# Performance work log

Measured on AMD Instinct MI355X. Metric: run time of the kernel, lower is better.

## Reference

```python
import jax, jax.numpy as jnp
import numpy as np

B, C, H, W = 2, 64, 256, 256
DN = ('NCHW', 'OIHW', 'NCHW')


def _conv1x1(x, w, b):
    # x: [B,C,H,W], w: [O,C,1,1]
    return jnp.einsum('bchw,oc->bohw', x, w[:, :, 0, 0]) + b[None, :, None, None]


def _dw3x3(x, w, b):
    # depthwise 3x3, padding=1, groups=C; w: [C,1,3,3]
    y = jax.lax.conv_general_dilated(x, w, (1, 1), [(1, 1), (1, 1)],
                                     feature_group_count=x.shape[1],
                                     dimension_numbers=DN)
    return y + b[None, :, None, None]


def _proj(x, w1, b1, w2, b2):
    return _dw3x3(_conv1x1(x, w1, b1), w2, b2)


def _pixel_attention(initial, pattn1, pa_w, pa_b):
    b, c, h, w = initial.shape
    # interleave channels: [x_c0, p_c0, x_c1, p_c1, ...] per 'b c t h w -> b (c t) h w'
    x2 = jnp.stack([initial, pattn1], axis=2).reshape(b, 2 * c, h, w)
    x2 = jnp.pad(x2, ((0, 0), (0, 0), (3, 3), (3, 3)), mode='reflect')
    y = jax.lax.conv_general_dilated(x2, pa_w, (1, 1), 'VALID',
                                     feature_group_count=c,
                                     dimension_numbers=DN)
    return jax.nn.sigmoid(y + pa_b[None, :, None, None])


def setup_inputs() -> dict:
    key = jax.random.key(0)
    ks = jax.random.split(key, 26)

    def n(k, shape, s=0.05):
        return jax.random.normal(k, shape, dtype=jnp.float32) * s

    d = {
        'x_l': jax.random.normal(ks[0], (B, C, H, W), dtype=jnp.float32),
        'x_r': jax.random.normal(ks[1], (B, C, H, W), dtype=jnp.float32),
    }
    i = 2
    for pfx in ('lp1', 'rp1', 'lp2', 'rp2'):
        d[pfx + '_w1'] = n(ks[i], (C, C, 1, 1)); i += 1
        d[pfx + '_b1'] = n(ks[i], (C,)); i += 1
        d[pfx + '_w2'] = n(ks[i], (C, 1, 3, 3)); i += 1
        d[pfx + '_b2'] = n(ks[i], (C,)); i += 1
    for pfx in ('lp3', 'rp3'):
        d[pfx + '_w'] = n(ks[i], (C, C, 1, 1)); i += 1
        d[pfx + '_b'] = n(ks[i], (C,)); i += 1
    d['pa_w'] = n(ks[i], (C, 2, 7, 7)); i += 1
    d['pa_b'] = n(ks[i], (C,))
    return d


def reference(x_l, x_r,
              lp1_w1, lp1_b1, lp1_w2, lp1_b2,
              rp1_w1, rp1_b1, rp1_w2, rp1_b2,
              lp2_w1, lp2_b1, lp2_w2, lp2_b2,
              rp2_w1, rp2_b1, rp2_w2, rp2_b2,
              lp3_w, lp3_b, rp3_w, rp3_b,
              pa_w, pa_b):
    c = x_l.shape[1]
    scale = c ** (-0.5)
    initial = x_l + x_r

    # projections (1x1 conv + depthwise 3x3), then move channels last: [B,H,W,C]
    Q_l = _proj(x_l, lp1_w1, lp1_b1, lp1_w2, lp1_b2).transpose(0, 2, 3, 1)
    Q_r = _proj(x_r, rp1_w1, rp1_b1, rp1_w2, rp1_b2).transpose(0, 2, 3, 1)
    V_l = _proj(x_l, lp2_w1, lp2_b1, lp2_w2, lp2_b2).transpose(0, 2, 3, 1)
    V_r = _proj(x_r, rp2_w1, rp2_b1, rp2_w2, rp2_b2).transpose(0, 2, 3, 1)

    # cross-attention along the width axis per spatial row: [B,H,W,W]
    attn = jnp.einsum('bhwc,bhvc->bhwv', Q_l, Q_r) * scale
    F_r2l = jnp.einsum('bhwv,bhvc->bhwc', jax.nn.softmax(attn, axis=-1), V_r)
    F_l2r = jnp.einsum('bhwv,bhwc->bhvc', jax.nn.softmax(attn, axis=2), V_l)

    F_r2l = _conv1x1(F_r2l.transpose(0, 3, 1, 2), lp3_w, lp3_b)
    F_l2r = _conv1x1(F_l2r.transpose(0, 3, 1, 2), rp3_w, rp3_b)

    # PixelAttention returns sigmoid(...); EAGFM applies sigmoid again (faithful)
    a = jax.nn.sigmoid(_pixel_attention(initial, F_l2r + F_r2l, pa_w, pa_b))
    return a * x_l + (1.0 - a) * x_r
```

## Files before the change

### kernel.cpp

```cpp
#include <hip/hip_runtime.h>

typedef unsigned int uint;
typedef unsigned short ushort;
typedef _Float16 h2 __attribute__((ext_vector_type(2)));
typedef _Float16 f16x8 __attribute__((ext_vector_type(8)));
typedef float f32x4 __attribute__((ext_vector_type(4)));

#define HW 65536
#define W_ 256
#define H_ 256
#define C_ 64

__device__ __forceinline__ ushort f2hu(float f) { union { ushort u; _Float16 h; } x; x.h = (_Float16)f; return x.u; }
__device__ __forceinline__ float hu2f(ushort u) { union { ushort u; _Float16 h; } x; x.u = u; return (float)x.h; }

#define MFMA16(a, b, c) __builtin_amdgcn_mfma_f32_16x16x32_f16((a), (b), (c), 0, 0, 0)

__global__ __launch_bounds__(256) void wconv_k(const float* __restrict__ a0, const float* __restrict__ a1,
                                               const float* __restrict__ a2, const float* __restrict__ a3,
                                               const float* __restrict__ a4, const float* __restrict__ a5,
                                               ushort* __restrict__ dst) {
    int m = blockIdx.x;
    const float* src = m == 0 ? a0 : m == 1 ? a1 : m == 2 ? a2 : m == 3 ? a3 : m == 4 ? a4 : a5;
    ushort* d = dst + m * 4096;
    for (int i = threadIdx.x; i < 4096; i += 256) d[i] = f2hu(src[i]);
}

__global__ __launch_bounds__(256) void wpat_k(const float* __restrict__ pw, ushort* __restrict__ tbl) {
    int c = blockIdx.x;
    for (int i = threadIdx.x; i < 7168; i += 256) {
        int j = i & 7;
        int lane = (i >> 3) & 63;
        int f = i >> 9;
        int arr = f < 7 ? 0 : 1;
        int dy = f < 7 ? f : f - 7;
        int l15 = lane & 15, quad = lane >> 4;
        int k = quad * 8 + j;
        int t = k - l15 - 1;
        float v = (t >= 0 && t < 7) ? pw[c * 98 + arr * 49 + dy * 7 + t] : 0.0f;
        tbl[c * 7168 + i] = f2hu(v);
    }
}

__global__ __launch_bounds__(256, 2) void c1d_k(const float* __restrict__ x,
                                                const ushort* __restrict__ wfA,
                                                const float* __restrict__ biasA,
                                                ushort* __restrict__ yA,
                                                const ushort* __restrict__ wfB,
                                                const float* __restrict__ biasB,
                                                ushort* __restrict__ yB) {
    __shared__ ushort sY[64 * 264];
    int tid = threadIdx.x;
    int wv = tid >> 6, lane = tid & 63;
    int l15 = lane & 15, quad = lane >> 4;
    int pix0 = blockIdx.x * 256;
    int b = pix0 >> 16, hw0 = pix0 & 65535;
    const float* xb = x + ((size_t)b << 22) + hw0;

    f16x8 aX[4][2];
#pragma unroll
    for (int mt = 0; mt < 4; ++mt) {
        int pixl = wv * 64 + mt * 16 + l15;
#pragma unroll
        for (int kc = 0; kc < 2; ++kc) {
            f16x8 a;
#pragma unroll
            for (int j = 0; j < 8; ++j) {
                int c = kc * 32 + quad * 8 + j;
                a[j] = (_Float16)xb[((size_t)c << 16) + pixl];
            }
            aX[mt][kc] = a;
        }
    }

    for (int mat = 0; mat < 2; ++mat) {
        const ushort* wf = mat == 0 ? wfA : wfB;
        const float* bias = mat == 0 ? biasA : biasB;
        ushort* y = mat == 0 ? yA : yB;

        f16x8 bW[4][2];
#pragma unroll
        for (int nt = 0; nt < 4; ++nt)
#pragma unroll
            for (int kc = 0; kc < 2; ++kc)
                bW[nt][kc] = *(const f16x8*)(wf + (nt * 16 + l15) * 64 + kc * 32 + quad * 8);

        f32x4 acc[4][4];
#pragma unroll
        for (int mt = 0; mt < 4; ++mt)
#pragma unroll
            for (int nt = 0; nt < 4; ++nt) {
                f32x4 s = (f32x4)(0.0f);
                s = MFMA16(aX[mt][0], bW[nt][0], s);
                s = MFMA16(aX[mt][1], bW[nt][1], s);
                acc[mt][nt] = s;
            }

        if (mat == 1) __syncthreads();
#pragma unroll
        for (int nt = 0; nt < 4; ++nt) {
            int o = nt * 16 + l15;
            float bv = bias[o];
#pragma unroll
            for (int mt = 0; mt < 4; ++mt) {
                int pixl = wv * 64 + mt * 16 + quad * 4;
#pragma unroll
                for (int r = 0; r < 4; r += 2) {
                    h2 hh;
                    hh.x = (_Float16)(acc[mt][nt][r] + bv);
                    hh.y = (_Float16)(acc[mt][nt][r + 1] + bv);
                    *(h2*)&sY[o * 264 + pixl + r] = hh;
                }
            }
        }
        __syncthreads();
        ushort* yb = y + ((((size_t)b << 16) + hw0 + tid) << 6);
#pragma unroll
        for (int g = 0; g < 8; ++g) {
            ushort vs[8];
#pragma unroll
            for (int k = 0; k < 8; ++k) vs[k] = sY[(g * 8 + k) * 264 + tid];
            uint4 o;
            o.x = (uint)vs[0] | ((uint)vs[1] << 16);
            o.y = (uint)vs[2] | ((uint)vs[3] << 16);
            o.z = (uint)vs[4] | ((uint)vs[5] << 16);
            o.w = (uint)vs[6] | ((uint)vs[7] << 16);
            *(uint4*)(yb + g * 8) = o;
        }
    }
}

__global__ __launch_bounds__(256) void dwq_k(const ushort* __restrict__ xcl,
                                             const float* __restrict__ wgt,
                                             const float* __restrict__ bias,
                                             ushort* __restrict__ out) {
    __shared__ float sW[576];
    int tid = threadIdx.x;
    for (int i = tid; i < 576; i += 256) sW[i] = wgt[i];
    __syncthreads();
    int c = tid & 63, wq = tid >> 6;
    int wt = blockIdx.x, h = blockIdx.y, b = blockIdx.z;
    int wbase = wt * 64 + wq * 16;
    const float* wp = sW + c * 9;
    float bv = bias[c];
    float acc[16];
#pragma unroll
    for (int i = 0; i < 16; ++i) acc[i] = bv;
    size_t plane = (size_t)b << 16;
#pragma unroll
    for (int r = 0; r < 3; ++r) {
        int hh = h - 1 + r;
        int hhc = hh < 0 ? 0 : (hh > 255 ? 255 : hh);
        bool okh = (hh >= 0 && hh <= 255);
        float w0t = wp[r * 3], w1t = wp[r * 3 + 1], w2t = wp[r * 3 + 2];
        float v[18];
#pragma unroll
        for (int t = 0; t < 18; ++t) {
            int ww = wbase - 1 + t;
            int wwc = ww < 0 ? 0 : (ww > 255 ? 255 : ww);
            float xv = hu2f(xcl[((plane + (size_t)hhc * 256 + wwc) << 6) + c]);
            v[t] = (okh && ww >= 0 && ww <= 255) ? xv : 0.0f;
        }
#pragma unroll
        for (int i = 0; i < 16; ++i)
            acc[i] += w0t * v[i] + w1t * v[i + 1] + w2t * v[i + 2];
    }
    size_t obase = ((plane + (size_t)h * 256 + wbase) << 6) + c;
#pragma unroll
    for (int i = 0; i < 16; ++i)
        out[obase + ((size_t)i << 6)] = f2hu(acc[i]);
}

__global__ __launch_bounds__(256) void dwv_k(const ushort* __restrict__ xcl,
                                             const float* __restrict__ wgt,
                                             const float* __restrict__ bias,
                                             ushort* __restrict__ out) {
    __shared__ float sW[576];
    __shared__ ushort sT[64 * 66];
    int tid = threadIdx.x;
    for (int i = tid; i < 576; i += 256) sW[i] = wgt[i];
    __syncthreads();
    int c = tid & 63, wq = tid >> 6;
    int wt = blockIdx.x, h = blockIdx.y, b = blockIdx.z;
    int wbase = wt * 64 + wq * 16;
    const float* wp = sW + c * 9;
    float bv = bias[c];
    float acc[16];
#pragma unroll
    for (int i = 0; i < 16; ++i) acc[i] = bv;
    size_t plane = (size_t)b << 16;
#pragma unroll
    for (int r = 0; r < 3; ++r) {
        int hh = h - 1 + r;
        int hhc = hh < 0 ? 0 : (hh > 255 ? 255 : hh);
        bool okh = (hh >= 0 && hh <= 255);
        float w0t = wp[r * 3], w1t = wp[r * 3 + 1], w2t = wp[r * 3 + 2];
        float v[18];
#pragma unroll
        for (int t = 0; t < 18; ++t) {
            int ww = wbase - 1 + t;
            int wwc = ww < 0 ? 0 : (ww > 255 ? 255 : ww);
            float xv = hu2f(xcl[((plane + (size_t)hhc * 256 + wwc) << 6) + c]);
            v[t] = (okh && ww >= 0 && ww <= 255) ? xv : 0.0f;
        }
#pragma unroll
        for (int i = 0; i < 16; ++i)
            acc[i] += w0t * v[i] + w1t * v[i + 1] + w2t * v[i + 2];
    }
#pragma unroll
    for (int i = 0; i < 16; i += 2) {
        h2 hh2;
        hh2.x = (_Float16)acc[i];
        hh2.y = (_Float16)acc[i + 1];
        *(h2*)&sT[c * 66 + wq * 16 + i] = hh2;
    }
    __syncthreads();
    int cr = tid >> 2, ch = tid & 3;
    uint vb[8];
#pragma unroll
    for (int k = 0; k < 8; ++k) vb[k] = *(const uint*)&sT[cr * 66 + ch * 16 + k * 2];
    uint4 o0, o1;
    o0.x = vb[0]; o0.y = vb[1]; o0.z = vb[2]; o0.w = vb[3];
    o1.x = vb[4]; o1.y = vb[5]; o1.z = vb[6]; o1.w = vb[7];
    size_t bh16 = ((size_t)b * 256 + h) * 16384;
    ushort* ob = out + bh16 + (size_t)cr * 256 + wt * 64 + ch * 16;
    *(uint4*)ob = o0;
    *(uint4*)(ob + 8) = o1;
}

__global__ __launch_bounds__(256, 2) void att2_k(const ushort* __restrict__ Ql,
                                                 const ushort* __restrict__ Qr,
                                                 const ushort* __restrict__ Vl,
                                                 const ushort* __restrict__ Vr,
                                                 ushort* __restrict__ Fr2l,
                                                 ushort* __restrict__ Fl2r) {
    int bh = blockIdx.x;
    int tid = threadIdx.x;
    int wv = tid >> 6, lane = tid & 63;
    int l15 = lane & 15, quad = lane >> 4;
    __shared__ ushort sE[256 * 72];
    __shared__ ushort sEt[64 * 264];

    const ushort* qlb = Ql + (size_t)bh * 16384;
    const ushort* qrb = Qr + (size_t)bh * 16384;
    const ushort* vlb = Vl + (size_t)bh * 16384;
    const ushort* vrb = Vr + (size_t)bh * 16384;
    int p0 = wv * 64;
    int c0 = wv * 16;

    f16x8 aQ[4][2];
#pragma unroll
    for (int mt = 0; mt < 4; ++mt)
#pragma unroll
        for (int kc = 0; kc < 2; ++kc)
            aQ[mt][kc] = *(const f16x8*)(qlb + (p0 + mt * 16 + l15) * 64 + kc * 32 + quad * 8);

    f16x8 onesf;
#pragma unroll
    for (int i = 0; i < 8; ++i) onesf[i] = (_Float16)1.0f;

    f32x4 num1[4][4];
    f32x4 den[4];
#pragma unroll
    for (int mt = 0; mt < 4; ++mt) {
        den[mt] = (f32x4)(0.0f);
#pragma unroll
        for (int nt = 0; nt < 4; ++nt) num1[mt][nt] = (f32x4)(0.0f);
    }

    for (int kt = 0; kt < 4; ++kt) {
        int k0 = kt * 64;
        f32x4 S[4][4];
#pragma unroll
        for (int nt = 0; nt < 4; ++nt) {
            f16x8 bQ[2];
#pragma unroll
            for (int kc = 0; kc < 2; ++kc)
                bQ[kc] = *(const f16x8*)(qrb + (k0 + nt * 16 + l15) * 64 + kc * 32 + quad * 8);
#pragma unroll
            for (int mt = 0; mt < 4; ++mt) {
                f32x4 s = (f32x4)(0.0f);
                s = MFMA16(aQ[mt][0], bQ[0], s);
                s = MFMA16(aQ[mt][1], bQ[1], s);
                S[mt][nt] = s;
            }
        }
#pragma unroll
        for (int mt = 0; mt < 4; ++mt)
#pragma unroll
            for (int nt = 0; nt < 4; ++nt)
#pragma unroll
                for (int r = 0; r < 4; ++r)
                    S[mt][nt][r] = __expf(S[mt][nt][r] * 0.125f);

        __syncthreads();
#pragma unroll
        for (int mt = 0; mt < 4; ++mt)
#pragma unroll
            for (int nt = 0; nt < 4; ++nt)
#pragma unroll
                for (int r = 0; r < 4; ++r)
                    sE[(p0 + mt * 16 + quad * 4 + r) * 72 + nt * 16 + l15] = f2hu(S[mt][nt][r]);
#pragma unroll
        for (int mt = 0; mt < 4; ++mt)
#pragma unroll
            for (int nt = 0; nt < 4; ++nt)
#pragma unroll
            for (int pr = 0; pr < 4; pr += 2) {
                h2 hh;
                hh.x = (_Float16)S[mt][nt][pr];
                hh.y = (_Float16)S[mt][nt][pr + 1];
                *(h2*)&sEt[(nt * 16 + l15) * 264 + p0 + mt * 16 + quad * 4 + pr] = hh;
            }
        __syncthreads();

        f16x8 aE[4][2];
#pragma unroll
        for (int mt = 0; mt < 4; ++mt)
#pragma unroll
            for (int kc = 0; kc < 2; ++kc)
                aE[mt][kc] = *(const f16x8*)&sE[(p0 + mt * 16 + l15) * 72 + kc * 32 + quad * 8];
#pragma unroll
        for (int mt = 0; mt < 4; ++mt) {
            den[mt] = MFMA16(aE[mt][0], onesf, den[mt]);
            den[mt] = MFMA16(aE[mt][1], onesf, den[mt]);
        }
#pragma unroll
        for (int nt = 0; nt < 4; ++nt) {
            f16x8 bV[2];
#pragma unroll
            for (int kc = 0; kc < 2; ++kc)
                bV[kc] = *(const f16x8*)(vrb + (nt * 16 + l15) * 256 + k0 + kc * 32 + quad * 8);
#pragma unroll
            for (int mt = 0; mt < 4; ++mt) {
                num1[mt][nt] = MFMA16(aE[mt][0], bV[0], num1[mt][nt]);
                num1[mt][nt] = MFMA16(aE[mt][1], bV[1], num1[mt][nt]);
            }
        }
        f32x4 num2[4], den2[4];
#pragma unroll
        for (int mt = 0; mt < 4; ++mt) { num2[mt] = (f32x4)(0.0f); den2[mt] = (f32x4)(0.0f); }
        for (int pc = 0; pc < 8; ++pc) {
            f16x8 bL = *(const f16x8*)(vlb + (c0 + l15) * 256 + pc * 32 + quad * 8);
#pragma unroll
            for (int mt = 0; mt < 4; ++mt) {
                f16x8 aT = *(const f16x8*)&sEt[(mt * 16 + l15) * 264 + pc * 32 + quad * 8];
                num2[mt] = MFMA16(aT, bL, num2[mt]);
                den2[mt] = MFMA16(aT, onesf, den2[mt]);
            }
        }
#pragma unroll
        for (int mt = 0; mt < 4; ++mt)
#pragma unroll
            for (int r = 0; r < 4; ++r) {
                float v = num2[mt][r] * (1.0f / den2[mt][r]);
                Fl2r[(size_t)bh * 16384 + (k0 + mt * 16 + quad * 4 + r) * 64 + c0 + l15] = f2hu(v);
            }
    }
#pragma unroll
    for (int mt = 0; mt < 4; ++mt)
#pragma unroll
        for (int r = 0; r < 4; ++r) {
            float inv = 1.0f / den[mt][r];
#pragma unroll
            for (int nt = 0; nt < 4; ++nt) {
                float v = num1[mt][nt][r] * inv;
                Fr2l[(size_t)bh * 16384 + (p0 + mt * 16 + quad * 4 + r) * 64 + nt * 16 + l15] = f2hu(v);
            }
        }
}

__global__ __launch_bounds__(256, 2) void p3m_k(const ushort* __restrict__ F1,
                                                const ushort* __restrict__ F2,
                                                const ushort* __restrict__ wf1,
                                                const float* __restrict__ b1,
                                                const ushort* __restrict__ wf2,
                                                const float* __restrict__ b2,
                                                ushort* __restrict__ outp) {
    __shared__ ushort sY[64 * 264];
    int tid = threadIdx.x;
    int wv = tid >> 6, lane = tid & 63;
    int l15 = lane & 15, quad = lane >> 4;
    int pix0 = blockIdx.x * 256;
    int b = pix0 >> 16, hw0 = pix0 & 65535;

    f32x4 acc[4][4];
#pragma unroll
    for (int mt = 0; mt < 4; ++mt)
#pragma unroll
        for (int nt = 0; nt < 4; ++nt) acc[mt][nt] = (f32x4)(0.0f);

    for (int mat = 0; mat < 2; ++mat) {
        const ushort* F = mat == 0 ? F1 : F2;
        const ushort* wf = mat == 0 ? wf1 : wf2;
        f16x8 aF[4][2], bW[4][2];
#pragma unroll
        for (int mt = 0; mt < 4; ++mt) {
            int pixg = pix0 + wv * 64 + mt * 16 + l15;
#pragma unroll
            for (int kc = 0; kc < 2; ++kc)
                aF[mt][kc] = *(const f16x8*)(F + (size_t)pixg * 64 + kc * 32 + quad * 8);
        }
#pragma unroll
        for (int nt = 0; nt < 4; ++nt)
#pragma unroll
            for (int kc = 0; kc < 2; ++kc)
                bW[nt][kc] = *(const f16x8*)(wf + (nt * 16 + l15) * 64 + kc * 32 + quad * 8);
#pragma unroll
        for (int mt = 0; mt < 4; ++mt)
#pragma unroll
            for (int nt = 0; nt < 4; ++nt) {
                acc[mt][nt] = MFMA16(aF[mt][0], bW[nt][0], acc[mt][nt]);
                acc[mt][nt] = MFMA16(aF[mt][1], bW[nt][1], acc[mt][nt]);
            }
    }

#pragma unroll
    for (int nt = 0; nt < 4; ++nt) {
        int o = nt * 16 + l15;
        float bv = b1[o] + b2[o];
#pragma unroll
        for (int mt = 0; mt < 4; ++mt) {
            int pixl = wv * 64 + mt * 16 + quad * 4;
#pragma unroll
            for (int r = 0; r < 4; r += 2) {
                h2 hh;
                hh.x = (_Float16)(acc[mt][nt][r] + bv);
                hh.y = (_Float16)(acc[mt][nt][r + 1] + bv);
                *(h2*)&sY[o * 264 + pixl + r] = hh;
            }
        }
    }
    __syncthreads();
    ushort* yb = outp + ((size_t)b << 22) + hw0;
#pragma unroll
    for (int i = 0; i < 16; ++i) {
        int o = wv * 16 + i;
        uint2 v = *(const uint2*)&sY[o * 264 + lane * 4];
        *(uint2*)(yb + ((size_t)o << 16) + lane * 4) = v;
    }
}

__global__ __launch_bounds__(256, 4) void p4m_k(const float* __restrict__ x_l,
                                                const float* __restrict__ x_r,
                                                const ushort* __restrict__ pt,
                                                const ushort* __restrict__ tbl,
                                                const float* __restrict__ pb,
                                                float* __restrict__ out) {
    __shared__ ushort s_t[22 * 320];
    __shared__ ushort p_t[22 * 320];
    int tid = threadIdx.x;
    int tile = blockIdx.x & 15;
    int bc = blockIdx.x >> 4;
    int c = bc & 63;
    int h0 = tile << 4;
    size_t cbase = (size_t)bc << 16;

    {
        int a = tid & 127, rr = tid >> 7;
        int k = 2 * a + 4;
        int slotbase = (k >> 3);
        for (int pass = 0; pass < 11; ++pass) {
            int row = pass * 2 + rr;
            int hh = h0 + row - 3;
            hh = hh < 0 ? -hh : (hh > 255 ? 510 - hh : hh);
            size_t rb = cbase + ((size_t)hh << 8);
            float2 xl2 = *(const float2*)(x_l + rb + 2 * a);
            float2 xr2 = *(const float2*)(x_r + rb + 2 * a);
            uint pv = *(const uint*)(pt + rb + 2 * a);
            h2 sh;
            sh.x = (_Float16)(xl2.x + xr2.x);
            sh.y = (_Float16)(xl2.y + xr2.y);
            int off = row * 320 + (((slotbase ^ (row & 7)) << 3) | (k & 7));
            *(h2*)&s_t[off] = sh;
            *(uint*)&p_t[off] = pv;
        }
    }
    if (tid < 176) {
        int row = tid >> 3, g = tid & 7;
        int k = g < 2 ? g * 2 : (g < 4 ? 260 + (g - 2) * 2 : 264 + (g - 4) * 2);
        h2 sh; uint pv;
        if (g < 4) {
            int hh = h0 + row - 3;
            hh = hh < 0 ? -hh : (hh > 255 ? 510 - hh : hh);
            size_t rb = cbase + ((size_t)hh << 8);
            int w0 = k - 4, w1 = k - 3;
            int s0 = w0 < 0 ? -w0 : (w0 > 255 ? 510 - w0 : w0);
            int s1 = w1 < 0 ? -w1 : (w1 > 255 ? 510 - w1 : w1);
            sh.x = (_Float16)(x_l[rb + s0] + x_r[rb + s0]);
            sh.y = (_Float16)(x_l[rb + s1] + x_r[rb + s1]);
            pv = (uint)pt[rb + s0] | ((uint)pt[rb + s1] << 16);
        } else {
            sh.x = (_Float16)0.0f; sh.y = (_Float16)0.0f;
            pv = 0;
        }
        int off = row * 320 + ((((k >> 3) ^ (row & 7)) << 3) | (k & 7));
        *(h2*)&s_t[off] = sh;
        *(uint*)&p_t[off] = pv;
    }

    int wv = tid >> 6, lane = tid & 63;
    int l15 = lane & 15, quad = lane >> 4;
    const ushort* tb = tbl + c * 7168;
    f16x8 bW[14];
#pragma unroll
    for (int f = 0; f < 14; ++f)
        bW[f] = *(const f16x8*)(tb + (f * 64 + lane) * 8);

    float bias = pb[c];
    f32x4 acc[4];
#pragma unroll
    for (int t = 0; t < 4; ++t) acc[t] = (f32x4)(bias);

    __syncthreads();

#pragma unroll
    for (int f = 0; f < 14; ++f) {
        int dy = f < 7 ? f : f - 7;
        const ushort* tp = f < 7 ? s_t : p_t;
        int row = l15 + dy;
        int rbase = row * 320;
        int rx = row & 7;
#pragma unroll
        for (int t = 0; t < 4; ++t) {
            int L = wv * 8 + 2 * t + quad;
            f16x8 aF = *(const f16x8*)&tp[rbase + ((L ^ rx) << 3)];
            acc[t] = MFMA16(aF, bW[f], acc[t]);
        }
    }

    int hrow = h0 + quad * 4;
#pragma unroll
    for (int t = 0; t < 4; ++t) {
        int w = wv * 64 + t * 16 + l15;
#pragma unroll
        for (int r = 0; r < 4; ++r) {
            size_t idx = cbase + (size_t)(hrow + r) * 256 + w;
            float z = acc[t][r];
            float s1 = 1.0f / (1.0f + __expf(-z));
            float a  = 1.0f / (1.0f + __expf(-s1));
            float xl = x_l[idx], xr = x_r[idx];
            out[idx] = xr + a * (xl - xr);
        }
    }
}

extern "C" void kernel_launch(void* const* d_in, const int* in_sizes, int n_in,
                              void* d_out, int out_size, void* d_ws, size_t ws_size,
                              hipStream_t stream) {
    const float* x_l = (const float*)d_in[0];
    const float* x_r = (const float*)d_in[1];
    const float* lp1_w1 = (const float*)d_in[2];
    const float* lp1_b1 = (const float*)d_in[3];
    const float* lp1_w2 = (const float*)d_in[4];
    const float* lp1_b2 = (const float*)d_in[5];
    const float* rp1_w1 = (const float*)d_in[6];
    const float* rp1_b1 = (const float*)d_in[7];
    const float* rp1_w2 = (const float*)d_in[8];
    const float* rp1_b2 = (const float*)d_in[9];
    const float* lp2_w1 = (const float*)d_in[10];
    const float* lp2_b1 = (const float*)d_in[11];
    const float* lp2_w2 = (const float*)d_in[12];
    const float* lp2_b2 = (const float*)d_in[13];
    const float* rp2_w1 = (const float*)d_in[14];
    const float* rp2_b1 = (const float*)d_in[15];
    const float* rp2_w2 = (const float*)d_in[16];
    const float* rp2_b2 = (const float*)d_in[17];
    const float* lp3_w = (const float*)d_in[18];
    const float* lp3_b = (const float*)d_in[19];
    const float* rp3_w = (const float*)d_in[20];
    const float* rp3_b = (const float*)d_in[21];
    const float* pa_w = (const float*)d_in[22];
    const float* pa_b = (const float*)d_in[23];

    const size_t N = (size_t)2 * 64 * 256 * 256;
    char* ws = (char*)d_ws;
    ushort* tmpA = (ushort*)ws;
    ushort* wf16 = (ushort*)(ws + N * 2);
    ushort* tbl  = (ushort*)(ws + N * 2 + 6 * 4096 * 2);
    ushort* q_l   = (ushort*)(ws + N * 4);
    ushort* q_r   = q_l + N;
    ushort* v_l   = q_r + N;
    ushort* v_r   = v_l + N;
    ushort* f_r2l = v_r + N;
    ushort* f_l2r = f_r2l + N;
    ushort* tmpB  = f_l2r + N;

    dim3 blk(256);
    dim3 g_c1(512);
    dim3 g_dw(4, 256, 2);
    dim3 g_att(512);
    dim3 g_p3(512);
    dim3 g_p4(2048);

    wconv_k<<<6, blk, 0, stream>>>(lp1_w1, rp1_w1, lp2_w1, rp2_w1, lp3_w, rp3_w, wf16);
    wpat_k<<<64, blk, 0, stream>>>(pa_w, tbl);

    c1d_k<<<g_c1, blk, 0, stream>>>(x_l, wf16 + 0 * 4096, lp1_b1, tmpA, wf16 + 2 * 4096, lp2_b1, tmpB);
    dwq_k<<<g_dw, blk, 0, stream>>>(tmpA, lp1_w2, lp1_b2, q_l);
    dwv_k<<<g_dw, blk, 0, stream>>>(tmpB, lp2_w2, lp2_b2, v_l);

    c1d_k<<<g_c1, blk, 0, stream>>>(x_r, wf16 + 1 * 4096, rp1_b1, tmpA, wf16 + 3 * 4096, rp2_b1, tmpB);
    dwq_k<<<g_dw, blk, 0, stream>>>(tmpA, rp1_w2, rp1_b2, q_r);
    dwv_k<<<g_dw, blk, 0, stream>>>(tmpB, rp2_w2, rp2_b2, v_r);

    att2_k<<<g_att, blk, 0, stream>>>(q_l, q_r, v_l, v_r, f_r2l, f_l2r);

    p3m_k<<<g_p3, blk, 0, stream>>>(f_r2l, f_l2r, wf16 + 4 * 4096, lp3_b, wf16 + 5 * 4096, rp3_b, tmpA);

    p4m_k<<<g_p4, blk, 0, stream>>>(x_l, x_r, tmpA, tbl, pa_b, (float*)d_out);
}
```

Measured before the change: 323.2 us.

## Merge left/right 1x1 conv launches and split attention over 8 waves

The two per-side 1x1 conv launches are merged into one kernel with a 2D grid. Each side now writes to its own scratch buffers, so the depthwise kernels no longer wait behind each other on shared temporaries. The attention kernel moves from 256 to 512 threads per block: each wave handles 32 query rows instead of 64, and the transpose-side V product is split across wave halves. This halves per-wave register pressure and raises parallelism, at the cost of more workspace and more waves sharing the same LDS tiles and barriers.

```diff
diff --git a/kernel.cpp b/kernel.cpp
--- a/kernel.cpp
+++ b/kernel.cpp
@@ -42,14 +42,23 @@
     }
 }
 
-__global__ __launch_bounds__(256, 2) void c1d_k(const float* __restrict__ x,
-                                                const ushort* __restrict__ wfA,
-                                                const float* __restrict__ biasA,
-                                                ushort* __restrict__ yA,
-                                                const ushort* __restrict__ wfB,
-                                                const float* __restrict__ biasB,
-                                                ushort* __restrict__ yB) {
+__global__ __launch_bounds__(256, 2) void c1df_k(const float* __restrict__ xl,
+                                                 const float* __restrict__ xr,
+                                                 const ushort* __restrict__ wf16,
+                                                 const float* __restrict__ bA0, const float* __restrict__ bB0,
+                                                 const float* __restrict__ bA1, const float* __restrict__ bB1,
+                                                 ushort* __restrict__ y0A, ushort* __restrict__ y0B,
+                                                 ushort* __restrict__ y1A, ushort* __restrict__ y1B) {
     __shared__ ushort sY[64 * 264];
+    int side = blockIdx.y;
+    const float* x = side ? xr : xl;
+    const ushort* wfA = wf16 + side * 4096;
+    const ushort* wfB = wf16 + (2 + side) * 4096;
+    const float* biasA = side ? bA1 : bA0;
+    const float* biasB = side ? bB1 : bB0;
+    ushort* yAo = side ? y1A : y0A;
+    ushort* yBo = side ? y1B : y0B;
+
     int tid = threadIdx.x;
     int wv = tid >> 6, lane = tid & 63;
     int l15 = lane & 15, quad = lane >> 4;
@@ -76,7 +85,7 @@
     for (int mat = 0; mat < 2; ++mat) {
         const ushort* wf = mat == 0 ? wfA : wfB;
         const float* bias = mat == 0 ? biasA : biasB;
-        ushort* y = mat == 0 ? yA : yB;
+        ushort* y = mat == 0 ? yAo : yBo;
 
         f16x8 bW[4][2];
 #pragma unroll
@@ -228,12 +237,12 @@
     *(uint4*)(ob + 8) = o1;
 }
 
-__global__ __launch_bounds__(256, 2) void att2_k(const ushort* __restrict__ Ql,
-                                                 const ushort* __restrict__ Qr,
-                                                 const ushort* __restrict__ Vl,
-                                                 const ushort* __restrict__ Vr,
-                                                 ushort* __restrict__ Fr2l,
-                                                 ushort* __restrict__ Fl2r) {
+__global__ __launch_bounds__(512, 2) void att2x_k(const ushort* __restrict__ Ql,
+                                                  const ushort* __restrict__ Qr,
+                                                  const ushort* __restrict__ Vl,
+                                                  const ushort* __restrict__ Vr,
+                                                  ushort* __restrict__ Fr2l,
+                                                  ushort* __restrict__ Fl2r) {
     int bh = blockIdx.x;
     int tid = threadIdx.x;
     int wv = tid >> 6, lane = tid & 63;
@@ -245,12 +254,14 @@
     const ushort* qrb = Qr + (size_t)bh * 16384;
     const ushort* vlb = Vl + (size_t)bh * 16384;
     const ushort* vrb = Vr + (size_t)bh * 16384;
-    int p0 = wv * 64;
-    int c0 = wv * 16;
-
-    f16x8 aQ[4][2];
-#pragma unroll
-    for (int mt = 0; mt < 4; ++mt)
+    int p0 = wv * 32;
+    int vh = wv >> 2;
+    int cq = wv & 3;
+    int c0 = cq * 16;
+
+    f16x8 aQ[2][2];
+#pragma unroll
+    for (int mt = 0; mt < 2; ++mt)
 #pragma unroll
         for (int kc = 0; kc < 2; ++kc)
             aQ[mt][kc] = *(const f16x8*)(qlb + (p0 + mt * 16 + l15) * 64 + kc * 32 + quad * 8);
@@ -259,10 +270,10 @@
 #pragma unroll
     for (int i = 0; i < 8; ++i) onesf[i] = (_Float16)1.0f;
 
-    f32x4 num1[4][4];
-    f32x4 den[4];
-#pragma unroll
-    for (int mt = 0; mt < 4; ++mt) {
+    f32x4 num1[2][4];
+    f32x4 den[2];
+#pragma unroll
+    for (int mt = 0; mt < 2; ++mt) {
         den[mt] = (f32x4)(0.0f);
 #pragma unroll
         for (int nt = 0; nt < 4; ++nt) num1[mt][nt] = (f32x4)(0.0f);
@@ -270,7 +281,7 @@
 
     for (int kt = 0; kt < 4; ++kt) {
         int k0 = kt * 64;
-        f32x4 S[4][4];
+        f32x4 S[2][4];
 #pragma unroll
         for (int nt = 0; nt < 4; ++nt) {
             f16x8 bQ[2];
@@ -278,7 +289,7 @@
             for (int kc = 0; kc < 2; ++kc)
                 bQ[kc] = *(const f16x8*)(qrb + (k0 + nt * 16 + l15) * 64 + kc * 32 + quad * 8);
 #pragma unroll
-            for (int mt = 0; mt < 4; ++mt) {
+            for (int mt = 0; mt < 2; ++mt) {
                 f32x4 s = (f32x4)(0.0f);
                 s = MFMA16(aQ[mt][0], bQ[0], s);
                 s = MFMA16(aQ[mt][1], bQ[1], s);
@@ -286,7 +297,7 @@
             }
         }
 #pragma unroll
-        for (int mt = 0; mt < 4; ++mt)
+        for (int mt = 0; mt < 2; ++mt)
 #pragma unroll
             for (int nt = 0; nt < 4; ++nt)
 #pragma unroll
@@ -295,14 +306,14 @@
 
         __syncthreads();
 #pragma unroll
-        for (int mt = 0; mt < 4; ++mt)
+        for (int mt = 0; mt < 2; ++mt)
 #pragma unroll
             for (int nt = 0; nt < 4; ++nt)
 #pragma unroll
                 for (int r = 0; r < 4; ++r)
                     sE[(p0 + mt * 16 + quad * 4 + r) * 72 + nt * 16 + l15] = f2hu(S[mt][nt][r]);
 #pragma unroll
-        for (int mt = 0; mt < 4; ++mt)
+        for (int mt = 0; mt < 2; ++mt)
 #pragma unroll
             for (int nt = 0; nt < 4; ++nt)
 #pragma unroll
@@ -314,14 +325,14 @@
             }
         __syncthreads();
 
-        f16x8 aE[4][2];
-#pragma unroll
-        for (int mt = 0; mt < 4; ++mt)
+        f16x8 aE[2][2];
+#pragma unroll
+        for (int mt = 0; mt < 2; ++mt)
 #pragma unroll
             for (int kc = 0; kc < 2; ++kc)
                 aE[mt][kc] = *(const f16x8*)&sE[(p0 + mt * 16 + l15) * 72 + kc * 32 + quad * 8];
 #pragma unroll
-        for (int mt = 0; mt < 4; ++mt) {
+        for (int mt = 0; mt < 2; ++mt) {
             den[mt] = MFMA16(aE[mt][0], onesf, den[mt]);
             den[mt] = MFMA16(aE[mt][1], onesf, den[mt]);
         }
@@ -332,33 +343,33 @@
             for (int kc = 0; kc < 2; ++kc)
                 bV[kc] = *(const f16x8*)(vrb + (nt * 16 + l15) * 256 + k0 + kc * 32 + quad * 8);
 #pragma unroll
-            for (int mt = 0; mt < 4; ++mt) {
+            for (int mt = 0; mt < 2; ++mt) {
                 num1[mt][nt] = MFMA16(aE[mt][0], bV[0], num1[mt][nt]);
                 num1[mt][nt] = MFMA16(aE[mt][1], bV[1], num1[mt][nt]);
             }
         }
-        f32x4 num2[4], den2[4];
-#pragma unroll
-        for (int mt = 0; mt < 4; ++mt) { num2[mt] = (f32x4)(0.0f); den2[mt] = (f32x4)(0.0f); }
+        f32x4 num2[2], den2[2];
+#pragma unroll
+        for (int mt = 0; mt < 2; ++mt) { num2[mt] = (f32x4)(0.0f); den2[mt] = (f32x4)(0.0f); }
         for (int pc = 0; pc < 8; ++pc) {
             f16x8 bL = *(const f16x8*)(vlb + (c0 + l15) * 256 + pc * 32 + quad * 8);
 #pragma unroll
-            for (int mt = 0; mt < 4; ++mt) {
-                f16x8 aT = *(const f16x8*)&sEt[(mt * 16 + l15) * 264 + pc * 32 + quad * 8];
+            for (int mt = 0; mt < 2; ++mt) {
+                f16x8 aT = *(const f16x8*)&sEt[(vh * 32 + mt * 16 + l15) * 264 + pc * 32 + quad * 8];
                 num2[mt] = MFMA16(aT, bL, num2[mt]);
                 den2[mt] = MFMA16(aT, onesf, den2[mt]);
             }
         }
 #pragma unroll
-        for (int mt = 0; mt < 4; ++mt)
+        for (int mt = 0; mt < 2; ++mt)
 #pragma unroll
             for (int r = 0; r < 4; ++r) {
                 float v = num2[mt][r] * (1.0f / den2[mt][r]);
-                Fl2r[(size_t)bh * 16384 + (k0 + mt * 16 + quad * 4 + r) * 64 + c0 + l15] = f2hu(v);
-            }
-    }
-#pragma unroll
-    for (int mt = 0; mt < 4; ++mt)
+                Fl2r[(size_t)bh * 16384 + (k0 + vh * 32 + mt * 16 + quad * 4 + r) * 64 + c0 + l15] = f2hu(v);
+            }
+    }
+#pragma unroll
+    for (int mt = 0; mt < 2; ++mt)
 #pragma unroll
         for (int r = 0; r < 4; ++r) {
             float inv = 1.0f / den[mt][r];
@@ -575,7 +586,7 @@
 
     const size_t N = (size_t)2 * 64 * 256 * 256;
     char* ws = (char*)d_ws;
-    ushort* tmpA = (ushort*)ws;
+    ushort* clA0 = (ushort*)ws;
     ushort* wf16 = (ushort*)(ws + N * 2);
     ushort* tbl  = (ushort*)(ws + N * 2 + 6 * 4096 * 2);
     ushort* q_l   = (ushort*)(ws + N * 4);
@@ -584,10 +595,12 @@
     ushort* v_r   = v_l + N;
     ushort* f_r2l = v_r + N;
     ushort* f_l2r = f_r2l + N;
-    ushort* tmpB  = f_l2r + N;
+    ushort* clB0  = f_l2r + N;
+    ushort* clA1  = clB0 + N;
+    ushort* clB1  = clA1 + N;
 
     dim3 blk(256);
-    dim3 g_c1(512);
+    dim3 g_c1(512, 2);
     dim3 g_dw(4, 256, 2);
     dim3 g_att(512);
     dim3 g_p3(512);
@@ -596,17 +609,17 @@
     wconv_k<<<6, blk, 0, stream>>>(lp1_w1, rp1_w1, lp2_w1, rp2_w1, lp3_w, rp3_w, wf16);
     wpat_k<<<64, blk, 0, stream>>>(pa_w, tbl);
 
-    c1d_k<<<g_c1, blk, 0, stream>>>(x_l, wf16 + 0 * 4096, lp1_b1, tmpA, wf16 + 2 * 4096, lp2_b1, tmpB);
-    dwq_k<<<g_dw, blk, 0, stream>>>(tmpA, lp1_w2, lp1_b2, q_l);
-    dwv_k<<<g_dw, blk, 0, stream>>>(tmpB, lp2_w2, lp2_b2, v_l);
-
-    c1d_k<<<g_c1, blk, 0, stream>>>(x_r, wf16 + 1 * 4096, rp1_b1, tmpA, wf16 + 3 * 4096, rp2_b1, tmpB);
-    dwq_k<<<g_dw, blk, 0, stream>>>(tmpA, rp1_w2, rp1_b2, q_r);
-    dwv_k<<<g_dw, blk, 0, stream>>>(tmpB, rp2_w2, rp2_b2, v_r);
-
-    att2_k<<<g_att, blk, 0, stream>>>(q_l, q_r, v_l, v_r, f_r2l, f_l2r);
-
-    p3m_k<<<g_p3, blk, 0, stream>>>(f_r2l, f_l2r, wf16 + 4 * 4096, lp3_b, wf16 + 5 * 4096, rp3_b, tmpA);
-
-    p4m_k<<<g_p4, blk, 0, stream>>>(x_l, x_r, tmpA, tbl, pa_b, (float*)d_out);
-}
+    c1df_k<<<g_c1, blk, 0, stream>>>(x_l, x_r, wf16,
+                                     lp1_b1, lp2_b1, rp1_b1, rp2_b1,
+                                     clA0, clB0, clA1, clB1);
+    dwq_k<<<g_dw, blk, 0, stream>>>(clA0, lp1_w2, lp1_b2, q_l);
+    dwq_k<<<g_dw, blk, 0, stream>>>(clA1, rp1_w2, rp1_b2, q_r);
+    dwv_k<<<g_dw, blk, 0, stream>>>(clB0, lp2_w2, lp2_b2, v_l);
+    dwv_k<<<g_dw, blk, 0, stream>>>(clB1, rp2_w2, rp2_b2, v_r);
+
+    att2x_k<<<g_att, dim3(512), 0, stream>>>(q_l, q_r, v_l, v_r, f_r2l, f_l2r);
+
+    p3m_k<<<g_p3, blk, 0, stream>>>(f_r2l, f_l2r, wf16 + 4 * 4096, lp3_b, wf16 + 5 * 4096, rp3_b, clA0);
+
+    p4m_k<<<g_p4, blk, 0, stream>>>(x_l, x_r, clA0, tbl, pa_b, (float*)d_out);
+}
```

Result: slower. 331.1 us (+2.4%).

## Merge left/right projection launches and compute four rows per depthwise block

Applied to the files above, without the earlier changes.

Combines the left and right 1x1 conv launches into one grid and the two depthwise launches into single kernels indexed by side. Each depthwise block now produces four output rows from six loaded input rows, reusing loaded rows across adjacent outputs. This aims to cut redundant global loads and launch overhead. It uses extra workspace buffers and more registers per thread.

```diff
diff --git a/kernel.cpp b/kernel.cpp
--- a/kernel.cpp
+++ b/kernel.cpp
@@ -42,14 +42,23 @@
     }
 }
 
-__global__ __launch_bounds__(256, 2) void c1d_k(const float* __restrict__ x,
-                                                const ushort* __restrict__ wfA,
-                                                const float* __restrict__ biasA,
-                                                ushort* __restrict__ yA,
-                                                const ushort* __restrict__ wfB,
-                                                const float* __restrict__ biasB,
-                                                ushort* __restrict__ yB) {
+__global__ __launch_bounds__(256, 2) void c1df_k(const float* __restrict__ xl,
+                                                 const float* __restrict__ xr,
+                                                 const ushort* __restrict__ wf16,
+                                                 const float* __restrict__ bA0, const float* __restrict__ bB0,
+                                                 const float* __restrict__ bA1, const float* __restrict__ bB1,
+                                                 ushort* __restrict__ y0A, ushort* __restrict__ y0B,
+                                                 ushort* __restrict__ y1A, ushort* __restrict__ y1B) {
     __shared__ ushort sY[64 * 264];
+    int side = blockIdx.y;
+    const float* x = side ? xr : xl;
+    const ushort* wfA = wf16 + side * 4096;
+    const ushort* wfB = wf16 + (2 + side) * 4096;
+    const float* biasA = side ? bA1 : bA0;
+    const float* biasB = side ? bB1 : bB0;
+    ushort* yAo = side ? y1A : y0A;
+    ushort* yBo = side ? y1B : y0B;
+
     int tid = threadIdx.x;
     int wv = tid >> 6, lane = tid & 63;
     int l15 = lane & 15, quad = lane >> 4;
@@ -76,7 +85,7 @@
     for (int mat = 0; mat < 2; ++mat) {
         const ushort* wf = mat == 0 ? wfA : wfB;
         const float* bias = mat == 0 ? biasA : biasB;
-        ushort* y = mat == 0 ? yA : yB;
+        ushort* y = mat == 0 ? yAo : yBo;
 
         f16x8 bW[4][2];
 #pragma unroll
@@ -130,29 +139,36 @@
     }
 }
 
-__global__ __launch_bounds__(256) void dwq_k(const ushort* __restrict__ xcl,
-                                             const float* __restrict__ wgt,
-                                             const float* __restrict__ bias,
-                                             ushort* __restrict__ out) {
+__global__ __launch_bounds__(256) void dwq2_k(const ushort* __restrict__ x0, const ushort* __restrict__ x1,
+                                              const float* __restrict__ w0, const float* __restrict__ w1,
+                                              const float* __restrict__ b0, const float* __restrict__ b1,
+                                              ushort* __restrict__ o0, ushort* __restrict__ o1) {
+    int z = blockIdx.z;
+    int side = z >> 1, b = z & 1;
+    const ushort* xcl = side ? x1 : x0;
+    const float* wgt = side ? w1 : w0;
+    const float* bias = side ? b1 : b0;
+    ushort* out = side ? o1 : o0;
     __shared__ float sW[576];
     int tid = threadIdx.x;
     for (int i = tid; i < 576; i += 256) sW[i] = wgt[i];
     __syncthreads();
     int c = tid & 63, wq = tid >> 6;
-    int wt = blockIdx.x, h = blockIdx.y, b = blockIdx.z;
+    int wt = blockIdx.x, h0 = blockIdx.y * 4;
     int wbase = wt * 64 + wq * 16;
     const float* wp = sW + c * 9;
     float bv = bias[c];
-    float acc[16];
-#pragma unroll
-    for (int i = 0; i < 16; ++i) acc[i] = bv;
+    float acc[4][16];
+#pragma unroll
+    for (int o = 0; o < 4; ++o)
+#pragma unroll
+        for (int i = 0; i < 16; ++i) acc[o][i] = bv;
     size_t plane = (size_t)b << 16;
 #pragma unroll
-    for (int r = 0; r < 3; ++r) {
-        int hh = h - 1 + r;
+    for (int r = 0; r < 6; ++r) {
+        int hh = h0 - 1 + r;
         int hhc = hh < 0 ? 0 : (hh > 255 ? 255 : hh);
         bool okh = (hh >= 0 && hh <= 255);
-        float w0t = wp[r * 3], w1t = wp[r * 3 + 1], w2t = wp[r * 3 + 2];
         float v[18];
 #pragma unroll
         for (int t = 0; t < 18; ++t) {
@@ -162,39 +178,56 @@
             v[t] = (okh && ww >= 0 && ww <= 255) ? xv : 0.0f;
         }
 #pragma unroll
+        for (int o = 0; o < 4; ++o) {
+            if (o >= r - 2 && o <= r) {
+                int wr = r - o;
+                float wa = wp[wr * 3], wb = wp[wr * 3 + 1], wc2 = wp[wr * 3 + 2];
+#pragma unroll
+                for (int i = 0; i < 16; ++i)
+                    acc[o][i] += wa * v[i] + wb * v[i + 1] + wc2 * v[i + 2];
+            }
+        }
+    }
+#pragma unroll
+    for (int o = 0; o < 4; ++o) {
+        size_t obase = ((plane + (size_t)(h0 + o) * 256 + wbase) << 6) + c;
+#pragma unroll
         for (int i = 0; i < 16; ++i)
-            acc[i] += w0t * v[i] + w1t * v[i + 1] + w2t * v[i + 2];
-    }
-    size_t obase = ((plane + (size_t)h * 256 + wbase) << 6) + c;
-#pragma unroll
-    for (int i = 0; i < 16; ++i)
-        out[obase + ((size_t)i << 6)] = f2hu(acc[i]);
-}
-
-__global__ __launch_bounds__(256) void dwv_k(const ushort* __restrict__ xcl,
-                                             const float* __restrict__ wgt,
-                                             const float* __restrict__ bias,
-                                             ushort* __restrict__ out) {
+            out[obase + ((size_t)i << 6)] = f2hu(acc[o][i]);
+    }
+}
+
+__global__ __launch_bounds__(256) void dwv2_k(const ushort* __restrict__ x0, const ushort* __restrict__ x1,
+                                              const float* __restrict__ w0, const float* __restrict__ w1,
+                                              const float* __restrict__ b0, const float* __restrict__ b1,
+                                              ushort* __restrict__ o0, ushort* __restrict__ o1) {
+    int z = blockIdx.z;
+    int side = z >> 1, b = z & 1;
+    const ushort* xcl = side ? x1 : x0;
+    const float* wgt = side ? w1 : w0;
+    const float* bias = side ? b1 : b0;
+    ushort* out = side ? o1 : o0;
     __shared__ float sW[576];
-    __shared__ ushort sT[64 * 66];
+    __shared__ ushort sT[4][64 * 66];
     int tid = threadIdx.x;
     for (int i = tid; i < 576; i += 256) sW[i] = wgt[i];
     __syncthreads();
     int c = tid & 63, wq = tid >> 6;
-    int wt = blockIdx.x, h = blockIdx.y, b = blockIdx.z;
+    int wt = blockIdx.x, h0 = blockIdx.y * 4;
     int wbase = wt * 64 + wq * 16;
     const float* wp = sW + c * 9;
     float bv = bias[c];
-    float acc[16];
-#pragma unroll
-    for (int i = 0; i < 16; ++i) acc[i] = bv;
+    float acc[4][16];
+#pragma unroll
+    for (int o = 0; o < 4; ++o)
+#pragma unroll
+        for (int i = 0; i < 16; ++i) acc[o][i] = bv;
     size_t plane = (size_t)b << 16;
 #pragma unroll
-    for (int r = 0; r < 3; ++r) {
-        int hh = h - 1 + r;
+    for (int r = 0; r < 6; ++r) {
+        int hh = h0 - 1 + r;
         int hhc = hh < 0 ? 0 : (hh > 255 ? 255 : hh);
         bool okh = (hh >= 0 && hh <= 255);
-        float w0t = wp[r * 3], w1t = wp[r * 3 + 1], w2t = wp[r * 3 + 2];
         float v[18];
 #pragma unroll
         for (int t = 0; t < 18; ++t) {
@@ -204,28 +237,40 @@
             v[t] = (okh && ww >= 0 && ww <= 255) ? xv : 0.0f;
         }
 #pragma unroll
-        for (int i = 0; i < 16; ++i)
-            acc[i] += w0t * v[i] + w1t * v[i + 1] + w2t * v[i + 2];
-    }
-#pragma unroll
-    for (int i = 0; i < 16; i += 2) {
-        h2 hh2;
-        hh2.x = (_Float16)acc[i];
-        hh2.y = (_Float16)acc[i + 1];
-        *(h2*)&sT[c * 66 + wq * 16 + i] = hh2;
-    }
+        for (int o = 0; o < 4; ++o) {
+            if (o >= r - 2 && o <= r) {
+                int wr = r - o;
+                float wa = wp[wr * 3], wb = wp[wr * 3 + 1], wc2 = wp[wr * 3 + 2];
+#pragma unroll
+                for (int i = 0; i < 16; ++i)
+                    acc[o][i] += wa * v[i] + wb * v[i + 1] + wc2 * v[i + 2];
+            }
+        }
+    }
+#pragma unroll
+    for (int o = 0; o < 4; ++o)
+#pragma unroll
+        for (int i = 0; i < 16; i += 2) {
+            h2 hh2;
+            hh2.x = (_Float16)acc[o][i];
+            hh2.y = (_Float16)acc[o][i + 1];
+            *(h2*)&sT[o][c * 66 + wq * 16 + i] = hh2;
+        }
     __syncthreads();
     int cr = tid >> 2, ch = tid & 3;
-    uint vb[8];
-#pragma unroll
-    for (int k = 0; k < 8; ++k) vb[k] = *(const uint*)&sT[cr * 66 + ch * 16 + k * 2];
-    uint4 o0, o1;
-    o0.x = vb[0]; o0.y = vb[1]; o0.z = vb[2]; o0.w = vb[3];
-    o1.x = vb[4]; o1.y = vb[5]; o1.z = vb[6]; o1.w = vb[7];
-    size_t bh16 = ((size_t)b * 256 + h) * 16384;
-    ushort* ob = out + bh16 + (size_t)cr * 256 + wt * 64 + ch * 16;
-    *(uint4*)ob = o0;
-    *(uint4*)(ob + 8) = o1;
+#pragma unroll
+    for (int o = 0; o < 4; ++o) {
+        uint vb[8];
+#pragma unroll
+        for (int k = 0; k < 8; ++k) vb[k] = *(const uint*)&sT[o][cr * 66 + ch * 16 + k * 2];
+        uint4 q0, q1;
+        q0.x = vb[0]; q0.y = vb[1]; q0.z = vb[2]; q0.w = vb[3];
+        q1.x = vb[4]; q1.y = vb[5]; q1.z = vb[6]; q1.w = vb[7];
+        size_t bh16 = ((size_t)b * 256 + h0 + o) * 16384;
+        ushort* ob = out + bh16 + (size_t)cr * 256 + wt * 64 + ch * 16;
+        *(uint4*)ob = q0;
+        *(uint4*)(ob + 8) = q1;
+    }
 }
 
 __global__ __launch_bounds__(256, 2) void att2_k(const ushort* __restrict__ Ql,
@@ -575,7 +620,7 @@
 
     const size_t N = (size_t)2 * 64 * 256 * 256;
     char* ws = (char*)d_ws;
-    ushort* tmpA = (ushort*)ws;
+    ushort* clA0 = (ushort*)ws;
     ushort* wf16 = (ushort*)(ws + N * 2);
     ushort* tbl  = (ushort*)(ws + N * 2 + 6 * 4096 * 2);
     ushort* q_l   = (ushort*)(ws + N * 4);
@@ -584,11 +629,13 @@
     ushort* v_r   = v_l + N;
     ushort* f_r2l = v_r + N;
     ushort* f_l2r = f_r2l + N;
-    ushort* tmpB  = f_l2r + N;
+    ushort* clB0  = f_l2r + N;
+    ushort* clA1  = clB0 + N;
+    ushort* clB1  = clA1 + N;
 
     dim3 blk(256);
-    dim3 g_c1(512);
-    dim3 g_dw(4, 256, 2);
+    dim3 g_c1(512, 2);
+    dim3 g_dw(4, 64, 4);
     dim3 g_att(512);
     dim3 g_p3(512);
     dim3 g_p4(2048);
@@ -596,17 +643,15 @@
     wconv_k<<<6, blk, 0, stream>>>(lp1_w1, rp1_w1, lp2_w1, rp2_w1, lp3_w, rp3_w, wf16);
     wpat_k<<<64, blk, 0, stream>>>(pa_w, tbl);
 
-    c1d_k<<<g_c1, blk, 0, stream>>>(x_l, wf16 + 0 * 4096, lp1_b1, tmpA, wf16 + 2 * 4096, lp2_b1, tmpB);
-    dwq_k<<<g_dw, blk, 0, stream>>>(tmpA, lp1_w2, lp1_b2, q_l);
-    dwv_k<<<g_dw, blk, 0, stream>>>(tmpB, lp2_w2, lp2_b2, v_l);
-
-    c1d_k<<<g_c1, blk, 0, stream>>>(x_r, wf16 + 1 * 4096, rp1_b1, tmpA, wf16 + 3 * 4096, rp2_b1, tmpB);
-    dwq_k<<<g_dw, blk, 0, stream>>>(tmpA, rp1_w2, rp1_b2, q_r);
-    dwv_k<<<g_dw, blk, 0, stream>>>(tmpB, rp2_w2, rp2_b2, v_r);
+    c1df_k<<<g_c1, blk, 0, stream>>>(x_l, x_r, wf16,
+                                     lp1_b1, lp2_b1, rp1_b1, rp2_b1,
+                                     clA0, clB0, clA1, clB1);
+    dwq2_k<<<g_dw, blk, 0, stream>>>(clA0, clA1, lp1_w2, rp1_w2, lp1_b2, rp1_b2, q_l, q_r);
+    dwv2_k<<<g_dw, blk, 0, stream>>>(clB0, clB1, lp2_w2, rp2_w2, lp2_b2, rp2_b2, v_l, v_r);
 
     att2_k<<<g_att, blk, 0, stream>>>(q_l, q_r, v_l, v_r, f_r2l, f_l2r);
 
-    p3m_k<<<g_p3, blk, 0, stream>>>(f_r2l, f_l2r, wf16 + 4 * 4096, lp3_b, wf16 + 5 * 4096, rp3_b, tmpA);
-
-    p4m_k<<<g_p4, blk, 0, stream>>>(x_l, x_r, tmpA, tbl, pa_b, (float*)d_out);
-}
+    p3m_k<<<g_p3, blk, 0, stream>>>(f_r2l, f_l2r, wf16 + 4 * 4096, lp3_b, wf16 + 5 * 4096, rp3_b, clA0);
+
+    p4m_k<<<g_p4, blk, 0, stream>>>(x_l, x_r, clA0, tbl, pa_b, (float*)d_out);
+}
```

Result: faster. 304.8 us (-5.7%).
